# Kernel optimization log

Measured on AMD Instinct MI355X. Metric: run time of the kernel, lower is better.

Reference implementation:

```python
import jax, jax.numpy as jnp
import numpy as np

N_NODES = 50000
N_EDGES = 800000
D = 128           # node feature / hidden / out_feature
E_FEAT = 16       # raw edge_attr dim
N_LAYERS = 3
BN_EPS = 1e-5
INV_SQRT2 = 0.7071067811865476


def setup_inputs() -> dict:
    key = jax.random.key(0)
    ks = jax.random.split(key, 12)
    x = jax.random.normal(ks[0], (N_NODES, D), dtype=jnp.float32)
    edge_index = jax.random.randint(ks[1], (2, N_EDGES), 0, N_NODES, dtype=jnp.int64)
    edge_attr = jax.random.normal(ks[2], (N_EDGES, E_FEAT), dtype=jnp.float32)
    edge_weight = jax.random.uniform(ks[3], (N_EDGES,), dtype=jnp.float32)
    # shared edge encoder (same module instance passed to every conv)
    We = jax.random.normal(ks[4], (E_FEAT, D), dtype=jnp.float32) * (1.0 / np.sqrt(E_FEAT))
    be = jnp.zeros((D,), dtype=jnp.float32)
    # per-layer MLP: Linear(D->D), GELU, Linear(D->D)
    W1 = jax.random.normal(ks[5], (N_LAYERS, D, D), dtype=jnp.float32) * (1.0 / np.sqrt(D))
    b1 = jnp.zeros((N_LAYERS, D), dtype=jnp.float32)
    W2 = jax.random.normal(ks[6], (N_LAYERS, D, D), dtype=jnp.float32) * (1.0 / np.sqrt(D))
    b2 = jnp.zeros((N_LAYERS, D), dtype=jnp.float32)
    eps = jnp.zeros((N_LAYERS,), dtype=jnp.float32)  # GINE eps params, init 0
    gamma = jnp.ones((N_LAYERS, D), dtype=jnp.float32)
    beta = jnp.zeros((N_LAYERS, D), dtype=jnp.float32)
    return {"x": x, "edge_index": edge_index, "edge_attr": edge_attr,
            "edge_weight": edge_weight, "We": We, "be": be, "W1": W1, "b1": b1,
            "W2": W2, "b2": b2, "eps": eps, "gamma": gamma, "beta": beta}


def reference(x, edge_index, edge_attr, edge_weight, We, be, W1, b1, W2, b2, eps, gamma, beta):
    src = edge_index[0]
    dst = edge_index[1]
    ew = edge_weight[:, None]                      # [E,1]
    edge_emb = edge_attr @ We + be                 # shared bond encoder, [E,D]
    n = x.shape[0]
    for i in range(N_LAYERS):
        # message: gelu(x_j + edge_emb) * edge_weight, scatter-add to dst
        m = jax.nn.gelu(x[src] + edge_emb, approximate=False) * ew   # [E,D]
        agg = jax.ops.segment_sum(m, dst, num_segments=n)            # [N,D]
        h = (1.0 + eps[i]) * x + agg
        h = jax.nn.gelu(h @ W1[i] + b1[i], approximate=False) @ W2[i] + b2[i]
        # BatchNorm1d, training mode (biased batch var)
        mu = jnp.mean(h, axis=0)
        var = jnp.var(h, axis=0)
        h = (h - mu) * jax.lax.rsqrt(var + BN_EPS) * gamma[i] + beta[i]
        h = jax.nn.gelu(h, approximate=False)
        # dropout p=0.0 -> identity; residual (shapes always match here)
        x = (x + h) * INV_SQRT2
    return x
```

## Files before the change

### kernel.cpp

```cpp
#include <hip/hip_runtime.h>
#include <math.h>

#define N_NODES 50000
#define N_EDGES 800000
#define D 128
#define E_FEAT 16
#define NLAYERS 3
#define BN_EPS 1e-5f
#define INV_SQRT2 0.70710678118654752f

typedef __attribute__((ext_vector_type(8))) short short8;
typedef __attribute__((ext_vector_type(4))) float f32x4;

__device__ __forceinline__ float gelu_fast(float v) {
    const float u = v * INV_SQRT2;
    const float a = __builtin_fabsf(u);
    const float t = __builtin_amdgcn_rcpf(__builtin_fmaf(0.3275911f, a, 1.0f));
    float p = __builtin_fmaf(1.061405429f, t, -1.453152027f);
    p = __builtin_fmaf(p, t, 1.421413741f);
    p = __builtin_fmaf(p, t, -0.284496736f);
    p = __builtin_fmaf(p, t, 0.254829592f);
    p = p * t;
    const float e = __builtin_amdgcn_exp2f(-1.4426950408889634f * a * a);
    const float erf_a = __builtin_fmaf(-p, e, 1.0f);
    const float erf_u = __builtin_copysignf(erf_a, u);
    return 0.5f * v * (1.0f + erf_u);
}

__device__ __forceinline__ unsigned short f2bf(float f) {
    unsigned u = __float_as_uint(f);
    unsigned r = (u + 0x7FFFu + ((u >> 16) & 1u)) >> 16;
    return (unsigned short)r;
}

__global__ __launch_bounds__(256) void count_kernel(const int* __restrict__ dst,
                                                    int* __restrict__ counts) {
    int e = blockIdx.x * 256 + threadIdx.x;
    if (e < N_EDGES) atomicAdd(&counts[dst[e]], 1);
}

#define NSCAN_BLOCKS 196
__global__ __launch_bounds__(256) void scan1_kernel(const int* __restrict__ counts,
                                                    int* __restrict__ offsets,
                                                    int* __restrict__ bsum) {
    __shared__ int wsum[4];
    __shared__ int wexcl[4];
    const int t = threadIdx.x, lane = t & 63, wid = t >> 6;
    const int idx = blockIdx.x * 256 + t;
    int v = (idx < N_NODES) ? counts[idx] : 0;
    int incl = v;
    #pragma unroll
    for (int off = 1; off < 64; off <<= 1) {
        int u = __shfl_up(incl, off, 64);
        if (lane >= off) incl += u;
    }
    if (lane == 63) wsum[wid] = incl;
    __syncthreads();
    if (t == 0) {
        int r = 0;
        #pragma unroll
        for (int g = 0; g < 4; ++g) { wexcl[g] = r; r += wsum[g]; }
        bsum[blockIdx.x] = r;
    }
    __syncthreads();
    if (idx < N_NODES) offsets[idx] = wexcl[wid] + (incl - v);
}

__global__ __launch_bounds__(256) void scan2_kernel(const int* __restrict__ bsum,
                                                    int* __restrict__ bbase,
                                                    int* __restrict__ offsets) {
    __shared__ int wsum[4];
    __shared__ int wexcl[4];
    const int t = threadIdx.x, lane = t & 63, wid = t >> 6;
    int v = (t < NSCAN_BLOCKS) ? bsum[t] : 0;
    int incl = v;
    #pragma unroll
    for (int off = 1; off < 64; off <<= 1) {
        int u = __shfl_up(incl, off, 64);
        if (lane >= off) incl += u;
    }
    if (lane == 63) wsum[wid] = incl;
    __syncthreads();
    if (t == 0) {
        int r = 0;
        #pragma unroll
        for (int g = 0; g < 4; ++g) { wexcl[g] = r; r += wsum[g]; }
        offsets[N_NODES] = r;
    }
    __syncthreads();
    if (t < NSCAN_BLOCKS) bbase[t] = wexcl[wid] + (incl - v);
}

__global__ __launch_bounds__(256) void scan3_kernel(int* __restrict__ offsets,
                                                    const int* __restrict__ bbase,
                                                    int* __restrict__ cursor) {
    const int idx = blockIdx.x * 256 + threadIdx.x;
    if (idx < N_NODES) {
        const int o = offsets[idx] + bbase[blockIdx.x];
        offsets[idx] = o;
        cursor[idx] = o;
    }
}

__global__ __launch_bounds__(256) void scatter_kernel(const int* __restrict__ dst,
                                                      int* __restrict__ cursor,
                                                      int* __restrict__ sorted_eid) {
    int e = blockIdx.x * 256 + threadIdx.x;
    if (e < N_EDGES) {
        int p = atomicAdd(&cursor[dst[e]], 1);
        sorted_eid[p] = e;
    }
}

__global__ __launch_bounds__(256) void permute_kernel(
    const int* __restrict__ sorted_eid,
    const int* __restrict__ src,
    const float* __restrict__ ew,
    const float* __restrict__ ea,
    int* __restrict__ sorted_src,
    float* __restrict__ sorted_ew,
    float* __restrict__ sorted_ea)
{
    int p = blockIdx.x * 256 + threadIdx.x;
    if (p < N_EDGES) {
        const int e = sorted_eid[p];
        sorted_src[p] = src[e];
        sorted_ew[p]  = ew[e];
        const float4* s4 = (const float4*)(ea + (size_t)e * E_FEAT);
        float4* d4 = (float4*)(sorted_ea + (size_t)p * E_FEAT);
        d4[0] = s4[0]; d4[1] = s4[1]; d4[2] = s4[2]; d4[3] = s4[3];
    }
}

__global__ __launch_bounds__(256) void pack_kernel(const float* __restrict__ W1,
                                                   const float* __restrict__ W2,
                                                   unsigned short* __restrict__ Wp) {
    const int idx = blockIdx.x * 256 + threadIdx.x;
    if (idx >= 6 * 2048) return;
    const int m    = idx >> 11;
    const int rem  = idx & 2047;
    const int ct   = rem >> 8;
    const int rem2 = rem & 255;
    const int kt   = rem2 >> 6;
    const int lane = rem2 & 63;
    const float* Wsrc = (m < 3) ? (W1 + (size_t)m * D * D)
                                : (W2 + (size_t)(m - 3) * D * D);
    const int k0  = kt * 32 + (lane >> 4) * 8;
    const int col = ct * 16 + (lane & 15);
    unsigned short o[8];
    #pragma unroll
    for (int j = 0; j < 8; ++j) o[j] = f2bf(Wsrc[(size_t)(k0 + j) * D + col]);
    unsigned short* d = Wp + (size_t)idx * 8;
    #pragma unroll
    for (int j = 0; j < 8; ++j) d[j] = o[j];
}

__global__ __launch_bounds__(256, 4) void aggregate_kernel(
    const float* __restrict__ x,
    const int* __restrict__ sorted_src,
    const float* __restrict__ sorted_ew,
    const float* __restrict__ sorted_ea,
    const int* __restrict__ offsets,
    const float* __restrict__ We,
    const float* __restrict__ be,
    const float* __restrict__ eps_p,
    float* __restrict__ pre)
{
    const int t = threadIdx.x;
    const int lane = t & 63;
    const int node = blockIdx.x * 4 + (t >> 6);
    const int c0 = lane * 2;

    float2 wreg[E_FEAT];
    #pragma unroll
    for (int k = 0; k < E_FEAT; ++k)
        wreg[k] = *(const float2*)&We[k * D + c0];
    const float2 bev = *(const float2*)&be[c0];
    const float e1 = 1.0f + *eps_p;

    const int start = __builtin_amdgcn_readfirstlane(offsets[node]);
    const int end   = __builtin_amdgcn_readfirstlane(offsets[node + 1]);

    float a0 = 0.0f, a1 = 0.0f;
    int p = start;
    for (; p + 2 <= end; p += 2) {
        const int s0 = __builtin_amdgcn_readfirstlane(sorted_src[p]);
        const int s1 = __builtin_amdgcn_readfirstlane(sorted_src[p + 1]);
        const float2 x0 = *(const float2*)&x[(size_t)s0 * D + c0];
        const float2 x1 = *(const float2*)&x[(size_t)s1 * D + c0];
        const float w0 = sorted_ew[p];
        const float w1 = sorted_ew[p + 1];
        const float* __restrict__ ea0 = sorted_ea + (size_t)p * E_FEAT;
        const float* __restrict__ ea1 = ea0 + E_FEAT;

        float m00 = bev.x, m01 = bev.y, m10 = bev.x, m11 = bev.y;
        #pragma unroll
        for (int k = 0; k < E_FEAT; ++k) {
            const float e0k = ea0[k];
            m00 = __builtin_fmaf(e0k, wreg[k].x, m00);
            m01 = __builtin_fmaf(e0k, wreg[k].y, m01);
        }
        #pragma unroll
        for (int k = 0; k < E_FEAT; ++k) {
            const float e1k = ea1[k];
            m10 = __builtin_fmaf(e1k, wreg[k].x, m10);
            m11 = __builtin_fmaf(e1k, wreg[k].y, m11);
        }
        a0 = __builtin_fmaf(gelu_fast(x0.x + m00), w0, a0);
        a1 = __builtin_fmaf(gelu_fast(x0.y + m01), w0, a1);
        a0 = __builtin_fmaf(gelu_fast(x1.x + m10), w1, a0);
        a1 = __builtin_fmaf(gelu_fast(x1.y + m11), w1, a1);
    }
    if (p < end) {
        const int s0 = __builtin_amdgcn_readfirstlane(sorted_src[p]);
        const float2 x0 = *(const float2*)&x[(size_t)s0 * D + c0];
        const float w0 = sorted_ew[p];
        const float* __restrict__ ea0 = sorted_ea + (size_t)p * E_FEAT;
        float m00 = bev.x, m01 = bev.y;
        #pragma unroll
        for (int k = 0; k < E_FEAT; ++k) {
            const float e0k = ea0[k];
            m00 = __builtin_fmaf(e0k, wreg[k].x, m00);
            m01 = __builtin_fmaf(e0k, wreg[k].y, m01);
        }
        a0 = __builtin_fmaf(gelu_fast(x0.x + m00), w0, a0);
        a1 = __builtin_fmaf(gelu_fast(x0.y + m01), w0, a1);
    }

    const float2 xnode = *(const float2*)&x[(size_t)node * D + c0];
    float2 o;
    o.x = e1 * xnode.x + a0;
    o.y = e1 * xnode.y + a1;
    *(float2*)&pre[(size_t)node * D + c0] = o;
}

#define GM 64
#define LDB 136

__global__ __launch_bounds__(256, 4) void mlp_fused_kernel(
    const float* __restrict__ pre,
    const unsigned short* __restrict__ Wp1,
    const float* __restrict__ b1,
    const unsigned short* __restrict__ Wp2,
    const float* __restrict__ b2,
    float* __restrict__ H,
    float* __restrict__ colsum,
    float* __restrict__ colsumsq)
{
    __shared__ __align__(16) unsigned short sAb[GM * LDB];
    __shared__ float sred[2][4][D];
    const int t = threadIdx.x;
    const int row0 = blockIdx.x * GM;

    for (int i = t; i < GM * (D / 4); i += 256) {
        const int r  = i / (D / 4);
        const int cc = (i % (D / 4)) * 4;
        const int gr = row0 + r;
        float4 v;
        if (gr < N_NODES) v = *(const float4*)&pre[(size_t)gr * D + cc];
        else { v.x = v.y = v.z = v.w = 0.0f; }
        ushort4 h;
        h.x = f2bf(v.x); h.y = f2bf(v.y); h.z = f2bf(v.z); h.w = f2bf(v.w);
        *(ushort4*)&sAb[r * LDB + cc] = h;
    }
    __syncthreads();

    const int wave = t >> 6, lane = t & 63;
    const int m0   = wave * 16;
    const int mrow = lane & 15;
    const int q    = lane >> 4;
    const int colb = lane & 15;

    short8 a[4];
    #pragma unroll
    for (int kt = 0; kt < 4; ++kt)
        a[kt] = *(const short8*)&sAb[(m0 + mrow) * LDB + kt * 32 + q * 8];

    f32x4 acc[8];
    #pragma unroll
    for (int ct = 0; ct < 8; ++ct) acc[ct] = (f32x4){0.f, 0.f, 0.f, 0.f};
    #pragma unroll
    for (int ct = 0; ct < 8; ++ct) {
        #pragma unroll
        for (int kt = 0; kt < 4; ++kt) {
            const short8 b = *(const short8*)&Wp1[((size_t)(ct * 4 + kt) * 64 + lane) * 8];
            acc[ct] = __builtin_amdgcn_mfma_f32_16x16x32_bf16(a[kt], b, acc[ct], 0, 0, 0);
        }
    }

    #pragma unroll
    for (int ct = 0; ct < 8; ++ct) {
        const float bb = b1[ct * 16 + colb];
        #pragma unroll
        for (int r = 0; r < 4; ++r) {
            const float o = gelu_fast(acc[ct][r] + bb);
            sAb[(m0 + q * 4 + r) * LDB + ct * 16 + colb] = f2bf(o);
        }
    }

    #pragma unroll
    for (int kt = 0; kt < 4; ++kt)
        a[kt] = *(const short8*)&sAb[(m0 + mrow) * LDB + kt * 32 + q * 8];
    #pragma unroll
    for (int ct = 0; ct < 8; ++ct) acc[ct] = (f32x4){0.f, 0.f, 0.f, 0.f};
    #pragma unroll
    for (int ct = 0; ct < 8; ++ct) {
        #pragma unroll
        for (int kt = 0; kt < 4; ++kt) {
            const short8 b = *(const short8*)&Wp2[((size_t)(ct * 4 + kt) * 64 + lane) * 8];
            acc[ct] = __builtin_amdgcn_mfma_f32_16x16x32_bf16(a[kt], b, acc[ct], 0, 0, 0);
        }
    }

    #pragma unroll
    for (int ct = 0; ct < 8; ++ct) {
        const float bb = b2[ct * 16 + colb];
        float ssum = 0.f, qsum = 0.f;
        #pragma unroll
        for (int r = 0; r < 4; ++r) {
            const int grow = row0 + m0 + q * 4 + r;
            const float o = acc[ct][r] + bb;
            if (grow < N_NODES) {
                H[(size_t)grow * D + ct * 16 + colb] = o;
                ssum += o;
                qsum += o * o;
            }
        }
        ssum += __shfl_xor(ssum, 16, 64);
        ssum += __shfl_xor(ssum, 32, 64);
        qsum += __shfl_xor(qsum, 16, 64);
        qsum += __shfl_xor(qsum, 32, 64);
        if (q == 0) {
            sred[0][wave][ct * 16 + colb] = ssum;
            sred[1][wave][ct * 16 + colb] = qsum;
        }
    }
    __syncthreads();
    if (t < D) {
        const float ss = sred[0][0][t] + sred[0][1][t] + sred[0][2][t] + sred[0][3][t];
        const float qq = sred[1][0][t] + sred[1][1][t] + sred[1][2][t] + sred[1][3][t];
        atomicAdd(&colsum[t], ss);
        atomicAdd(&colsumsq[t], qq);
    }
}

__global__ __launch_bounds__(256) void bn_apply_kernel(
    const float* __restrict__ H,
    const float* __restrict__ colsum,
    const float* __restrict__ colsumsq,
    const float* __restrict__ gamma,
    const float* __restrict__ beta,
    const float* __restrict__ x_in,
    float* __restrict__ x_out)
{
    const int idx = blockIdx.x * 256 + threadIdx.x;
    const int c0 = (idx & 31) * 4;
    const float invN = 1.0f / (float)N_NODES;

    const float4 s  = *(const float4*)&colsum[c0];
    const float4 q  = *(const float4*)&colsumsq[c0];
    const float4 g  = *(const float4*)&gamma[c0];
    const float4 bt = *(const float4*)&beta[c0];
    const float4 h  = *(const float4*)&H[(size_t)idx * 4];
    const float4 xv = *(const float4*)&x_in[(size_t)idx * 4];

    float4 o;
    {
        float mu = s.x * invN, var = q.x * invN - mu * mu;
        float hn = (h.x - mu) * rsqrtf(var + BN_EPS) * g.x + bt.x;
        o.x = (xv.x + gelu_fast(hn)) * INV_SQRT2;
    }
    {
        float mu = s.y * invN, var = q.y * invN - mu * mu;
        float hn = (h.y - mu) * rsqrtf(var + BN_EPS) * g.y + bt.y;
        o.y = (xv.y + gelu_fast(hn)) * INV_SQRT2;
    }
    {
        float mu = s.z * invN, var = q.z * invN - mu * mu;
        float hn = (h.z - mu) * rsqrtf(var + BN_EPS) * g.z + bt.z;
        o.z = (xv.z + gelu_fast(hn)) * INV_SQRT2;
    }
    {
        float mu = s.w * invN, var = q.w * invN - mu * mu;
        float hn = (h.w - mu) * rsqrtf(var + BN_EPS) * g.w + bt.w;
        o.w = (xv.w + gelu_fast(hn)) * INV_SQRT2;
    }
    *(float4*)&x_out[(size_t)idx * 4] = o;
}

extern "C" void kernel_launch(void* const* d_in, const int* in_sizes, int n_in,
                              void* d_out, int out_size, void* d_ws, size_t ws_size,
                              hipStream_t stream) {
    const float* x_in  = (const float*)d_in[0];
    const int*   ei    = (const int*)d_in[1];
    const float* ea    = (const float*)d_in[2];
    const float* ew    = (const float*)d_in[3];
    const float* We    = (const float*)d_in[4];
    const float* be    = (const float*)d_in[5];
    const float* W1    = (const float*)d_in[6];
    const float* b1    = (const float*)d_in[7];
    const float* W2    = (const float*)d_in[8];
    const float* b2    = (const float*)d_in[9];
    const float* eps   = (const float*)d_in[10];
    const float* gamma = (const float*)d_in[11];
    const float* beta  = (const float*)d_in[12];

    const int* src = ei;
    const int* dst = ei + N_EDGES;

    float* xcur = (float*)d_out;

    int*   counts       = (int*)d_ws;
    float* colsum_all   = (float*)(counts + N_NODES);
    float* colsumsq_all = colsum_all + NLAYERS * D;
    int*   cursor       = (int*)(colsumsq_all + NLAYERS * D);
    int*   offsets      = cursor + N_NODES;
    int*   bsum         = offsets + N_NODES + 4;
    int*   bbase        = bsum + 256;
    int*   sorted_eid   = bbase + 256;
    int*   sorted_src   = sorted_eid + N_EDGES;
    float* sorted_ew    = (float*)(sorted_src + N_EDGES);
    float* sorted_ea    = sorted_ew + N_EDGES;
    unsigned short* Wpack = (unsigned short*)(sorted_ea + (size_t)N_EDGES * E_FEAT);
    float* preH         = (float*)(Wpack + 6 * 2048 * 8);

    hipMemsetAsync(counts, 0, sizeof(int) * (N_NODES + 2 * NLAYERS * D), stream);
    count_kernel<<<(N_EDGES + 255) / 256, 256, 0, stream>>>(dst, counts);
    scan1_kernel<<<NSCAN_BLOCKS, 256, 0, stream>>>(counts, offsets, bsum);
    scan2_kernel<<<1, 256, 0, stream>>>(bsum, bbase, offsets);
    scan3_kernel<<<NSCAN_BLOCKS, 256, 0, stream>>>(offsets, bbase, cursor);
    scatter_kernel<<<(N_EDGES + 255) / 256, 256, 0, stream>>>(dst, cursor, sorted_eid);
    permute_kernel<<<(N_EDGES + 255) / 256, 256, 0, stream>>>(
        sorted_eid, src, ew, ea, sorted_src, sorted_ew, sorted_ea);
    pack_kernel<<<48, 256, 0, stream>>>(W1, W2, Wpack);

    const int mlp_blocks = (N_NODES + GM - 1) / GM;
    const int bn_blocks  = (N_NODES * D / 4) / 256;
    const int agg_blocks = N_NODES / 4;

    for (int i = 0; i < NLAYERS; ++i) {
        const float* xl = (i == 0) ? x_in : xcur;
        aggregate_kernel<<<agg_blocks, 256, 0, stream>>>(
            xl, sorted_src, sorted_ew, sorted_ea, offsets, We, be, eps + i, preH);
        mlp_fused_kernel<<<mlp_blocks, 256, 0, stream>>>(
            preH, Wpack + (size_t)i * 16384, b1 + (size_t)i * D,
            Wpack + (size_t)(3 + i) * 16384, b2 + (size_t)i * D,
            preH, colsum_all + i * D, colsumsq_all + i * D);
        bn_apply_kernel<<<bn_blocks, 256, 0, stream>>>(
            preH, colsum_all + i * D, colsumsq_all + i * D,
            gamma + (size_t)i * D, beta + (size_t)i * D, xl, xcur);
    }
}
```

Baseline: 687.0 us.

## Precompute fp16 edge embeddings once and reuse across layers in aggregation

Adds a kernel that computes the shared edge encoder output once per edge in sorted order and stores it as packed fp16, and a lighter aggregation kernel that reads these embeddings instead of recomputing the 16-wide projection every layer. It removes the per-layer edge matmul FMAs and the sorted edge_attr copy, and raises the occupancy hint. In exchange, each layer reads a 128-wide fp16 embedding per edge instead of 16 floats, which adds memory traffic, and fp16 storage reduces precision. The path is only taken when the workspace is large enough.

```diff
diff --git a/kernel.cpp b/kernel.cpp
--- a/kernel.cpp
+++ b/kernel.cpp
@@ -11,6 +11,9 @@
 
 typedef __attribute__((ext_vector_type(8))) short short8;
 typedef __attribute__((ext_vector_type(4))) float f32x4;
+typedef __fp16 fp16x2 __attribute__((ext_vector_type(2)));
+
+union H2U { fp16x2 h; unsigned u; };
 
 __device__ __forceinline__ float gelu_fast(float v) {
     const float u = v * INV_SQRT2;
@@ -119,17 +122,196 @@
     const float* __restrict__ ea,
     int* __restrict__ sorted_src,
     float* __restrict__ sorted_ew,
-    float* __restrict__ sorted_ea)
+    float* __restrict__ sorted_ea,
+    int copy_ea)
 {
     int p = blockIdx.x * 256 + threadIdx.x;
     if (p < N_EDGES) {
         const int e = sorted_eid[p];
         sorted_src[p] = src[e];
         sorted_ew[p]  = ew[e];
-        const float4* s4 = (const float4*)(ea + (size_t)e * E_FEAT);
-        float4* d4 = (float4*)(sorted_ea + (size_t)p * E_FEAT);
-        d4[0] = s4[0]; d4[1] = s4[1]; d4[2] = s4[2]; d4[3] = s4[3];
-    }
+        if (copy_ea) {
+            const float4* s4 = (const float4*)(ea + (size_t)e * E_FEAT);
+            float4* d4 = (float4*)(sorted_ea + (size_t)p * E_FEAT);
+            d4[0] = s4[0]; d4[1] = s4[1]; d4[2] = s4[2]; d4[3] = s4[3];
+        }
+    }
+}
+
+#define EMB_EPW 32
+__global__ __launch_bounds__(256, 4) void emb_kernel(
+    const int* __restrict__ sorted_eid,
+    const float* __restrict__ ea,
+    const float* __restrict__ We,
+    const float* __restrict__ be,
+    unsigned* __restrict__ emb)
+{
+    const int t = threadIdx.x, lane = t & 63;
+    const int wid = blockIdx.x * 4 + (t >> 6);
+    const int c0 = lane * 2;
+
+    float2 wreg[E_FEAT];
+    #pragma unroll
+    for (int k = 0; k < E_FEAT; ++k)
+        wreg[k] = *(const float2*)&We[k * D + c0];
+    const float2 bev = *(const float2*)&be[c0];
+
+    const int p0 = wid * EMB_EPW;
+    for (int p = p0; p < p0 + EMB_EPW; p += 2) {
+        const int e0 = __builtin_amdgcn_readfirstlane(sorted_eid[p]);
+        const int e1 = __builtin_amdgcn_readfirstlane(sorted_eid[p + 1]);
+        const float* __restrict__ ea0 = ea + (size_t)e0 * E_FEAT;
+        const float* __restrict__ ea1 = ea + (size_t)e1 * E_FEAT;
+        float m00 = bev.x, m01 = bev.y, m10 = bev.x, m11 = bev.y;
+        #pragma unroll
+        for (int k = 0; k < E_FEAT; ++k) {
+            const float v = ea0[k];
+            m00 = __builtin_fmaf(v, wreg[k].x, m00);
+            m01 = __builtin_fmaf(v, wreg[k].y, m01);
+        }
+        #pragma unroll
+        for (int k = 0; k < E_FEAT; ++k) {
+            const float v = ea1[k];
+            m10 = __builtin_fmaf(v, wreg[k].x, m10);
+            m11 = __builtin_fmaf(v, wreg[k].y, m11);
+        }
+        H2U cv0; cv0.h = __builtin_amdgcn_cvt_pkrtz(m00, m01);
+        H2U cv1; cv1.h = __builtin_amdgcn_cvt_pkrtz(m10, m11);
+        emb[(size_t)p * 64 + lane]       = cv0.u;
+        emb[(size_t)(p + 1) * 64 + lane] = cv1.u;
+    }
+}
+
+__global__ __launch_bounds__(256, 8) void aggregate_emb_kernel(
+    const float* __restrict__ x,
+    const int* __restrict__ sorted_src,
+    const float* __restrict__ sorted_ew,
+    const unsigned* __restrict__ emb,
+    const int* __restrict__ offsets,
+    const float* __restrict__ eps_p,
+    float* __restrict__ pre)
+{
+    const int t = threadIdx.x;
+    const int lane = t & 63;
+    const int node = blockIdx.x * 4 + (t >> 6);
+    const int c0 = lane * 2;
+    const float e1 = 1.0f + *eps_p;
+
+    const int start = __builtin_amdgcn_readfirstlane(offsets[node]);
+    const int end   = __builtin_amdgcn_readfirstlane(offsets[node + 1]);
+
+    float a0 = 0.0f, a1 = 0.0f;
+    int p = start;
+    for (; p + 2 <= end; p += 2) {
+        const int s0 = __builtin_amdgcn_readfirstlane(sorted_src[p]);
+        const int s1 = __builtin_amdgcn_readfirstlane(sorted_src[p + 1]);
+        const float2 x0 = *(const float2*)&x[(size_t)s0 * D + c0];
+        const float2 x1 = *(const float2*)&x[(size_t)s1 * D + c0];
+        const unsigned u0 = emb[(size_t)p * 64 + lane];
+        const unsigned u1 = emb[(size_t)(p + 1) * 64 + lane];
+        const float w0 = sorted_ew[p];
+        const float w1 = sorted_ew[p + 1];
+        H2U cv0; cv0.u = u0;
+        H2U cv1; cv1.u = u1;
+        a0 = __builtin_fmaf(gelu_fast(x0.x + (float)cv0.h[0]), w0, a0);
+        a1 = __builtin_fmaf(gelu_fast(x0.y + (float)cv0.h[1]), w0, a1);
+        a0 = __builtin_fmaf(gelu_fast(x1.x + (float)cv1.h[0]), w1, a0);
+        a1 = __builtin_fmaf(gelu_fast(x1.y + (float)cv1.h[1]), w1, a1);
+    }
+    if (p < end) {
+        const int s0 = __builtin_amdgcn_readfirstlane(sorted_src[p]);
+        const float2 x0 = *(const float2*)&x[(size_t)s0 * D + c0];
+        const unsigned u0 = emb[(size_t)p * 64 + lane];
+        const float w0 = sorted_ew[p];
+        H2U cv0; cv0.u = u0;
+        a0 = __builtin_fmaf(gelu_fast(x0.x + (float)cv0.h[0]), w0, a0);
+        a1 = __builtin_fmaf(gelu_fast(x0.y + (float)cv0.h[1]), w0, a1);
+    }
+
+    const float2 xnode = *(const float2*)&x[(size_t)node * D + c0];
+    float2 o;
+    o.x = e1 * xnode.x + a0;
+    o.y = e1 * xnode.y + a1;
+    *(float2*)&pre[(size_t)node * D + c0] = o;
+}
+
+__global__ __launch_bounds__(256, 4) void aggregate_kernel(
+    const float* __restrict__ x,
+    const int* __restrict__ sorted_src,
+    const float* __restrict__ sorted_ew,
+    const float* __restrict__ sorted_ea,
+    const int* __restrict__ offsets,
+    const float* __restrict__ We,
+    const float* __restrict__ be,
+    const float* __restrict__ eps_p,
+    float* __restrict__ pre)
+{
+    const int t = threadIdx.x;
+    const int lane = t & 63;
+    const int node = blockIdx.x * 4 + (t >> 6);
+    const int c0 = lane * 2;
+
+    float2 wreg[E_FEAT];
+    #pragma unroll
+    for (int k = 0; k < E_FEAT; ++k)
+        wreg[k] = *(const float2*)&We[k * D + c0];
+    const float2 bev = *(const float2*)&be[c0];
+    const float e1 = 1.0f + *eps_p;
+
+    const int start = __builtin_amdgcn_readfirstlane(offsets[node]);
+    const int end   = __builtin_amdgcn_readfirstlane(offsets[node + 1]);
+
+    float a0 = 0.0f, a1 = 0.0f;
+    int p = start;
+    for (; p + 2 <= end; p += 2) {
+        const int s0 = __builtin_amdgcn_readfirstlane(sorted_src[p]);
+        const int s1 = __builtin_amdgcn_readfirstlane(sorted_src[p + 1]);
+        const float2 x0 = *(const float2*)&x[(size_t)s0 * D + c0];
+        const float2 x1 = *(const float2*)&x[(size_t)s1 * D + c0];
+        const float w0 = sorted_ew[p];
+        const float w1 = sorted_ew[p + 1];
+        const float* __restrict__ ea0 = sorted_ea + (size_t)p * E_FEAT;
+        const float* __restrict__ ea1 = ea0 + E_FEAT;
+
+        float m00 = bev.x, m01 = bev.y, m10 = bev.x, m11 = bev.y;
+        #pragma unroll
+        for (int k = 0; k < E_FEAT; ++k) {
+            const float e0k = ea0[k];
+            m00 = __builtin_fmaf(e0k, wreg[k].x, m00);
+            m01 = __builtin_fmaf(e0k, wreg[k].y, m01);
+        }
+        #pragma unroll
+        for (int k = 0; k < E_FEAT; ++k) {
+            const float e1k = ea1[k];
+            m10 = __builtin_fmaf(e1k, wreg[k].x, m10);
+            m11 = __builtin_fmaf(e1k, wreg[k].y, m11);
+        }
+        a0 = __builtin_fmaf(gelu_fast(x0.x + m00), w0, a0);
+        a1 = __builtin_fmaf(gelu_fast(x0.y + m01), w0, a1);
+        a0 = __builtin_fmaf(gelu_fast(x1.x + m10), w1, a0);
+        a1 = __builtin_fmaf(gelu_fast(x1.y + m11), w1, a1);
+    }
+    if (p < end) {
+        const int s0 = __builtin_amdgcn_readfirstlane(sorted_src[p]);
+        const float2 x0 = *(const float2*)&x[(size_t)s0 * D + c0];
+        const float w0 = sorted_ew[p];
+        const float* __restrict__ ea0 = sorted_ea + (size_t)p * E_FEAT;
+        float m00 = bev.x, m01 = bev.y;
+        #pragma unroll
+        for (int k = 0; k < E_FEAT; ++k) {
+            const float e0k = ea0[k];
+            m00 = __builtin_fmaf(e0k, wreg[k].x, m00);
+            m01 = __builtin_fmaf(e0k, wreg[k].y, m01);
+        }
+        a0 = __builtin_fmaf(gelu_fast(x0.x + m00), w0, a0);
+        a1 = __builtin_fmaf(gelu_fast(x0.y + m01), w0, a1);
+    }
+
+    const float2 xnode = *(const float2*)&x[(size_t)node * D + c0];
+    float2 o;
+    o.x = e1 * xnode.x + a0;
+    o.y = e1 * xnode.y + a1;
+    *(float2*)&pre[(size_t)node * D + c0] = o;
 }
 
 __global__ __launch_bounds__(256) void pack_kernel(const float* __restrict__ W1,
@@ -155,85 +337,6 @@
     for (int j = 0; j < 8; ++j) d[j] = o[j];
 }
 
-__global__ __launch_bounds__(256, 4) void aggregate_kernel(
-    const float* __restrict__ x,
-    const int* __restrict__ sorted_src,
-    const float* __restrict__ sorted_ew,
-    const float* __restrict__ sorted_ea,
-    const int* __restrict__ offsets,
-    const float* __restrict__ We,
-    const float* __restrict__ be,
-    const float* __restrict__ eps_p,
-    float* __restrict__ pre)
-{
-    const int t = threadIdx.x;
-    const int lane = t & 63;
-    const int node = blockIdx.x * 4 + (t >> 6);
-    const int c0 = lane * 2;
-
-    float2 wreg[E_FEAT];
-    #pragma unroll
-    for (int k = 0; k < E_FEAT; ++k)
-        wreg[k] = *(const float2*)&We[k * D + c0];
-    const float2 bev = *(const float2*)&be[c0];
-    const float e1 = 1.0f + *eps_p;
-
-    const int start = __builtin_amdgcn_readfirstlane(offsets[node]);
-    const int end   = __builtin_amdgcn_readfirstlane(offsets[node + 1]);
-
-    float a0 = 0.0f, a1 = 0.0f;
-    int p = start;
-    for (; p + 2 <= end; p += 2) {
-        const int s0 = __builtin_amdgcn_readfirstlane(sorted_src[p]);
-        const int s1 = __builtin_amdgcn_readfirstlane(sorted_src[p + 1]);
-        const float2 x0 = *(const float2*)&x[(size_t)s0 * D + c0];
-        const float2 x1 = *(const float2*)&x[(size_t)s1 * D + c0];
-        const float w0 = sorted_ew[p];
-        const float w1 = sorted_ew[p + 1];
-        const float* __restrict__ ea0 = sorted_ea + (size_t)p * E_FEAT;
-        const float* __restrict__ ea1 = ea0 + E_FEAT;
-
-        float m00 = bev.x, m01 = bev.y, m10 = bev.x, m11 = bev.y;
-        #pragma unroll
-        for (int k = 0; k < E_FEAT; ++k) {
-            const float e0k = ea0[k];
-            m00 = __builtin_fmaf(e0k, wreg[k].x, m00);
-            m01 = __builtin_fmaf(e0k, wreg[k].y, m01);
-        }
-        #pragma unroll
-        for (int k = 0; k < E_FEAT; ++k) {
-            const float e1k = ea1[k];
-            m10 = __builtin_fmaf(e1k, wreg[k].x, m10);
-            m11 = __builtin_fmaf(e1k, wreg[k].y, m11);
-        }
-        a0 = __builtin_fmaf(gelu_fast(x0.x + m00), w0, a0);
-        a1 = __builtin_fmaf(gelu_fast(x0.y + m01), w0, a1);
-        a0 = __builtin_fmaf(gelu_fast(x1.x + m10), w1, a0);
-        a1 = __builtin_fmaf(gelu_fast(x1.y + m11), w1, a1);
-    }
-    if (p < end) {
-        const int s0 = __builtin_amdgcn_readfirstlane(sorted_src[p]);
-        const float2 x0 = *(const float2*)&x[(size_t)s0 * D + c0];
-        const float w0 = sorted_ew[p];
-        const float* __restrict__ ea0 = sorted_ea + (size_t)p * E_FEAT;
-        float m00 = bev.x, m01 = bev.y;
-        #pragma unroll
-        for (int k = 0; k < E_FEAT; ++k) {
-            const float e0k = ea0[k];
-            m00 = __builtin_fmaf(e0k, wreg[k].x, m00);
-            m01 = __builtin_fmaf(e0k, wreg[k].y, m01);
-        }
-        a0 = __builtin_fmaf(gelu_fast(x0.x + m00), w0, a0);
-        a1 = __builtin_fmaf(gelu_fast(x0.y + m01), w0, a1);
-    }
-
-    const float2 xnode = *(const float2*)&x[(size_t)node * D + c0];
-    float2 o;
-    o.x = e1 * xnode.x + a0;
-    o.y = e1 * xnode.y + a1;
-    *(float2*)&pre[(size_t)node * D + c0] = o;
-}
-
 #define GM 64
 #define LDB 136
 
@@ -423,6 +526,11 @@
     float* sorted_ea    = sorted_ew + N_EDGES;
     unsigned short* Wpack = (unsigned short*)(sorted_ea + (size_t)N_EDGES * E_FEAT);
     float* preH         = (float*)(Wpack + 6 * 2048 * 8);
+    unsigned* emb       = (unsigned*)(preH + (size_t)N_NODES * D);
+
+    const size_t needed = (size_t)((unsigned char*)(emb + (size_t)N_EDGES * 64)
+                                   - (unsigned char*)d_ws);
+    const int use_emb = (ws_size >= needed) ? 1 : 0;
 
     hipMemsetAsync(counts, 0, sizeof(int) * (N_NODES + 2 * NLAYERS * D), stream);
     count_kernel<<<(N_EDGES + 255) / 256, 256, 0, stream>>>(dst, counts);
@@ -431,7 +539,11 @@
     scan3_kernel<<<NSCAN_BLOCKS, 256, 0, stream>>>(offsets, bbase, cursor);
     scatter_kernel<<<(N_EDGES + 255) / 256, 256, 0, stream>>>(dst, cursor, sorted_eid);
     permute_kernel<<<(N_EDGES + 255) / 256, 256, 0, stream>>>(
-        sorted_eid, src, ew, ea, sorted_src, sorted_ew, sorted_ea);
+        sorted_eid, src, ew, ea, sorted_src, sorted_ew, sorted_ea, use_emb ? 0 : 1);
+    if (use_emb) {
+        emb_kernel<<<N_EDGES / (EMB_EPW * 4), 256, 0, stream>>>(
+            sorted_eid, ea, We, be, emb);
+    }
     pack_kernel<<<48, 256, 0, stream>>>(W1, W2, Wpack);
 
     const int mlp_blocks = (N_NODES + GM - 1) / GM;
@@ -440,8 +552,13 @@
 
     for (int i = 0; i < NLAYERS; ++i) {
         const float* xl = (i == 0) ? x_in : xcur;
-        aggregate_kernel<<<agg_blocks, 256, 0, stream>>>(
-            xl, sorted_src, sorted_ew, sorted_ea, offsets, We, be, eps + i, preH);
+        if (use_emb) {
+            aggregate_emb_kernel<<<agg_blocks, 256, 0, stream>>>(
+                xl, sorted_src, sorted_ew, emb, offsets, eps + i, preH);
+        } else {
+            aggregate_kernel<<<agg_blocks, 256, 0, stream>>>(
+                xl, sorted_src, sorted_ew, sorted_ea, offsets, We, be, eps + i, preH);
+        }
         mlp_fused_kernel<<<mlp_blocks, 256, 0, stream>>>(
             preH, Wpack + (size_t)i * 16384, b1 + (size_t)i * D,
             Wpack + (size_t)(3 + i) * 16384, b2 + (size_t)i * D,
```

Result: no change. 690.1 us (+0.5%).

## Split each node's edge aggregation across four waves with LDS reduction

Applied to the files above, without the earlier changes.

The aggregation kernel now gives each node its own 256-thread block. The four wavefronts take interleaved edges and combine their partial sums through shared memory, where before one wavefront handled a whole node. The goal is more memory-level parallelism per node, shorter per-wave dependency chains, and better balance for high-degree nodes, with occupancy raised to 8 blocks via launch bounds. In exchange it adds a __syncthreads, an LDS reduction and four times as many blocks, and each wave redundantly loads the We registers.

```diff
diff --git a/kernel.cpp b/kernel.cpp
--- a/kernel.cpp
+++ b/kernel.cpp
@@ -132,6 +132,78 @@
     }
 }
 
+#define AGG_BODY(P) do {                                                      \
+    const int s_ = __builtin_amdgcn_readfirstlane(sorted_src[P]);             \
+    const float2 xv_ = *(const float2*)&x[(size_t)s_ * D + c0];               \
+    const float w_ = sorted_ew[P];                                            \
+    const float* __restrict__ ea_ = sorted_ea + (size_t)(P) * E_FEAT;         \
+    float m0_ = bev.x, m1_ = bev.y;                                           \
+    _Pragma("unroll")                                                         \
+    for (int k = 0; k < E_FEAT; ++k) {                                        \
+        const float e_ = ea_[k];                                              \
+        m0_ = __builtin_fmaf(e_, wreg[k].x, m0_);                             \
+        m1_ = __builtin_fmaf(e_, wreg[k].y, m1_);                             \
+    }                                                                         \
+    a0 = __builtin_fmaf(gelu_fast(xv_.x + m0_), w_, a0);                      \
+    a1 = __builtin_fmaf(gelu_fast(xv_.y + m1_), w_, a1);                      \
+} while (0)
+
+__global__ __launch_bounds__(256, 8) void aggregate_kernel(
+    const float* __restrict__ x,
+    const int* __restrict__ sorted_src,
+    const float* __restrict__ sorted_ew,
+    const float* __restrict__ sorted_ea,
+    const int* __restrict__ offsets,
+    const float* __restrict__ We,
+    const float* __restrict__ be,
+    const float* __restrict__ eps_p,
+    float* __restrict__ pre)
+{
+    __shared__ float2 sacc[4][64];
+    const int t = threadIdx.x;
+    const int lane = t & 63;
+    const int w = t >> 6;
+    const int node = blockIdx.x;
+    const int c0 = lane * 2;
+
+    float2 wreg[E_FEAT];
+    #pragma unroll
+    for (int k = 0; k < E_FEAT; ++k)
+        wreg[k] = *(const float2*)&We[k * D + c0];
+    #pragma unroll
+    for (int k = 0; k < E_FEAT; ++k)
+        asm volatile("" : "+v"(wreg[k].x), "+v"(wreg[k].y));
+    const float2 bev = *(const float2*)&be[c0];
+
+    const int start = __builtin_amdgcn_readfirstlane(offsets[node]);
+    const int end   = __builtin_amdgcn_readfirstlane(offsets[node + 1]);
+
+    float a0 = 0.0f, a1 = 0.0f;
+    int p = start + w;
+    for (; p + 4 < end; p += 8) {
+        AGG_BODY(p);
+        AGG_BODY(p + 4);
+    }
+    if (p < end) AGG_BODY(p);
+
+    sacc[w][lane].x = a0;
+    sacc[w][lane].y = a1;
+    __syncthreads();
+
+    if (w == 0) {
+        const float2 r0 = sacc[0][lane];
+        const float2 r1 = sacc[1][lane];
+        const float2 r2 = sacc[2][lane];
+        const float2 r3 = sacc[3][lane];
+        const float e1 = 1.0f + *eps_p;
+        const float2 xnode = *(const float2*)&x[(size_t)node * D + c0];
+        float2 o;
+        o.x = __builtin_fmaf(e1, xnode.x, (r0.x + r1.x) + (r2.x + r3.x));
+        o.y = __builtin_fmaf(e1, xnode.y, (r0.y + r1.y) + (r2.y + r3.y));
+        *(float2*)&pre[(size_t)node * D + c0] = o;
+    }
+}
+
 __global__ __launch_bounds__(256) void pack_kernel(const float* __restrict__ W1,
                                                    const float* __restrict__ W2,
                                                    unsigned short* __restrict__ Wp) {
@@ -153,85 +225,6 @@
     unsigned short* d = Wp + (size_t)idx * 8;
     #pragma unroll
     for (int j = 0; j < 8; ++j) d[j] = o[j];
-}
-
-__global__ __launch_bounds__(256, 4) void aggregate_kernel(
-    const float* __restrict__ x,
-    const int* __restrict__ sorted_src,
-    const float* __restrict__ sorted_ew,
-    const float* __restrict__ sorted_ea,
-    const int* __restrict__ offsets,
-    const float* __restrict__ We,
-    const float* __restrict__ be,
-    const float* __restrict__ eps_p,
-    float* __restrict__ pre)
-{
-    const int t = threadIdx.x;
-    const int lane = t & 63;
-    const int node = blockIdx.x * 4 + (t >> 6);
-    const int c0 = lane * 2;
-
-    float2 wreg[E_FEAT];
-    #pragma unroll
-    for (int k = 0; k < E_FEAT; ++k)
-        wreg[k] = *(const float2*)&We[k * D + c0];
-    const float2 bev = *(const float2*)&be[c0];
-    const float e1 = 1.0f + *eps_p;
-
-    const int start = __builtin_amdgcn_readfirstlane(offsets[node]);
-    const int end   = __builtin_amdgcn_readfirstlane(offsets[node + 1]);
-
-    float a0 = 0.0f, a1 = 0.0f;
-    int p = start;
-    for (; p + 2 <= end; p += 2) {
-        const int s0 = __builtin_amdgcn_readfirstlane(sorted_src[p]);
-        const int s1 = __builtin_amdgcn_readfirstlane(sorted_src[p + 1]);
-        const float2 x0 = *(const float2*)&x[(size_t)s0 * D + c0];
-        const float2 x1 = *(const float2*)&x[(size_t)s1 * D + c0];
-        const float w0 = sorted_ew[p];
-        const float w1 = sorted_ew[p + 1];
-        const float* __restrict__ ea0 = sorted_ea + (size_t)p * E_FEAT;
-        const float* __restrict__ ea1 = ea0 + E_FEAT;
-
-        float m00 = bev.x, m01 = bev.y, m10 = bev.x, m11 = bev.y;
-        #pragma unroll
-        for (int k = 0; k < E_FEAT; ++k) {
-            const float e0k = ea0[k];
-            m00 = __builtin_fmaf(e0k, wreg[k].x, m00);
-            m01 = __builtin_fmaf(e0k, wreg[k].y, m01);
-        }
-        #pragma unroll
-        for (int k = 0; k < E_FEAT; ++k) {
-            const float e1k = ea1[k];
-            m10 = __builtin_fmaf(e1k, wreg[k].x, m10);
-            m11 = __builtin_fmaf(e1k, wreg[k].y, m11);
-        }
-        a0 = __builtin_fmaf(gelu_fast(x0.x + m00), w0, a0);
-        a1 = __builtin_fmaf(gelu_fast(x0.y + m01), w0, a1);
-        a0 = __builtin_fmaf(gelu_fast(x1.x + m10), w1, a0);
-        a1 = __builtin_fmaf(gelu_fast(x1.y + m11), w1, a1);
-    }
-    if (p < end) {
-        const int s0 = __builtin_amdgcn_readfirstlane(sorted_src[p]);
-        const float2 x0 = *(const float2*)&x[(size_t)s0 * D + c0];
-        const float w0 = sorted_ew[p];
-        const float* __restrict__ ea0 = sorted_ea + (size_t)p * E_FEAT;
-        float m00 = bev.x, m01 = bev.y;
-        #pragma unroll
-        for (int k = 0; k < E_FEAT; ++k) {
-            const float e0k = ea0[k];
-            m00 = __builtin_fmaf(e0k, wreg[k].x, m00);
-            m01 = __builtin_fmaf(e0k, wreg[k].y, m01);
-        }
-        a0 = __builtin_fmaf(gelu_fast(x0.x + m00), w0, a0);
-        a1 = __builtin_fmaf(gelu_fast(x0.y + m01), w0, a1);
-    }
-
-    const float2 xnode = *(const float2*)&x[(size_t)node * D + c0];
-    float2 o;
-    o.x = e1 * xnode.x + a0;
-    o.y = e1 * xnode.y + a1;
-    *(float2*)&pre[(size_t)node * D + c0] = o;
 }
 
 #define GM 64
@@ -436,11 +429,10 @@
 
     const int mlp_blocks = (N_NODES + GM - 1) / GM;
     const int bn_blocks  = (N_NODES * D / 4) / 256;
-    const int agg_blocks = N_NODES / 4;
 
     for (int i = 0; i < NLAYERS; ++i) {
         const float* xl = (i == 0) ? x_in : xcur;
-        aggregate_kernel<<<agg_blocks, 256, 0, stream>>>(
+        aggregate_kernel<<<N_NODES, 256, 0, stream>>>(
             xl, sorted_src, sorted_ew, sorted_ea, offsets, We, be, eps + i, preH);
         mlp_fused_kernel<<<mlp_blocks, 256, 0, stream>>>(
             preH, Wpack + (size_t)i * 16384, b1 + (size_t)i * D,
```

Measured after the change: 1.261 ms. 83.5% more time.
